# Kernel tuning notes

Hardware: AMD Instinct MI355X
Metric: run time of the kernel (lower is better)

## Reference

```python
import jax, jax.numpy as jnp
import numpy as np

DIM = 128
HEADS = 4
HEAD_DIM = DIM // HEADS
WS = (8, 8)
N = WS[0] * WS[1]
B = 4096
SCALE = HEAD_DIM ** -0.5


def _relative_position_index():
    # Swin-style relative position index, [N, N] int
    ch = np.arange(WS[0]); cw = np.arange(WS[1])
    coords = np.stack(np.meshgrid(ch, cw, indexing='ij'))          # [2, ws0, ws1]
    flat = coords.reshape(2, -1)                                    # [2, N]
    rel = flat[:, :, None] - flat[:, None, :]                       # [2, N, N]
    rel = rel.transpose(1, 2, 0)                                    # [N, N, 2]
    rel[:, :, 0] += WS[0] - 1
    rel[:, :, 1] += WS[1] - 1
    rel[:, :, 0] *= 2 * WS[1] - 1
    return jnp.asarray(rel.sum(-1))

REL_IDX = _relative_position_index()


def setup_inputs() -> dict:
    key = jax.random.key(0)
    ks = jax.random.split(key, 16)
    def lin(k, din, dout):
        return jax.random.normal(k, (din, dout), jnp.float32) * (din ** -0.5)
    return {
        'x': jax.random.normal(ks[0], (B, N, DIM), jnp.float32),
        'f': jax.random.normal(ks[1], (B, N, DIM), jnp.float32),
        'wq': lin(ks[2], DIM, DIM), 'bq': jnp.zeros((DIM,), jnp.float32),
        'wkv': lin(ks[3], DIM, 2 * DIM), 'bkv': jnp.zeros((2 * DIM,), jnp.float32),
        'wq_f': lin(ks[4], DIM, DIM), 'bq_f': jnp.zeros((DIM,), jnp.float32),
        'wkv_f': lin(ks[5], DIM, 2 * DIM), 'bkv_f': jnp.zeros((2 * DIM,), jnp.float32),
        'bias_table': jax.random.normal(ks[6], ((2 * WS[0] - 1) * (2 * WS[1] - 1), HEADS), jnp.float32) * 0.02,
        'wproj': lin(ks[7], DIM, DIM), 'bproj': jnp.zeros((DIM,), jnp.float32),
    }


def _qkv(t, wq, bq, wkv, bkv):
    Bn, Nn, C = t.shape
    q = (t @ wq + bq).reshape(Bn, Nn, HEADS, HEAD_DIM).transpose(0, 2, 1, 3)   # [B,H,N,D]
    kv = (t @ wkv + bkv).reshape(Bn, Nn, 2, HEADS, HEAD_DIM).transpose(2, 0, 3, 1, 4)
    return q, kv[0], kv[1]


def reference(x, f, wq, bq, wkv, bkv, wq_f, bq_f, wkv_f, bkv_f, bias_table, wproj, bproj):
    q, k, v = _qkv(x, wq, bq, wkv, bkv)
    attn = jnp.einsum('bhnd,bhmd->bhnm', q * SCALE, k)              # [B,H,N,N]
    q_f, k_f, _ = _qkv(f, wq_f, bq_f, wkv_f, bkv_f)
    attn_f = jnp.einsum('bhnd,bhmd->bhnm', q_f * SCALE, k_f)

    bias = bias_table[REL_IDX.reshape(-1)].reshape(N, N, HEADS)     # gather
    bias = bias.transpose(2, 0, 1)                                   # [H,N,N]
    ratio = attn.shape[-1] // bias.shape[-1]
    if ratio > 1:  # repeat last axis (no-op here since N == ws0*ws1)
        bias = jnp.repeat(bias, ratio, axis=-1)

    attn = (attn + bias[None]) * (attn_f + bias[None])               # joint modulation
    attn = jax.nn.softmax(attn, axis=-1)
    out = jnp.einsum('bhnm,bhmd->bhnd', attn, v)                     # [B,H,N,D]
    out = out.transpose(0, 2, 1, 3).reshape(x.shape[0], N, DIM)
    return out @ wproj + bproj
```

## Files before the change

### kernel.cpp

```cpp
#include <hip/hip_runtime.h>

typedef unsigned short u16;
typedef _Float16  f16x8  __attribute__((ext_vector_type(8)));
typedef _Float16  f16x4  __attribute__((ext_vector_type(4)));
typedef float     f32x4  __attribute__((ext_vector_type(4)));

#define MFMA_F16(a,b,c)  __builtin_amdgcn_mfma_f32_16x16x32_f16(a,b,c,0,0,0)

#define NTOK 64
#define DIM_ 128
#define SCALE_ 0.17677669529663687f

__device__ __forceinline__ u16 f2h_u(float x) {
    _Float16 h = (_Float16)x;
    return __builtin_bit_cast(u16, h);
}

__global__ void wja_prep(const float* __restrict__ wq, const float* __restrict__ wkv,
                         const float* __restrict__ wq_f, const float* __restrict__ wkv_f,
                         const float* __restrict__ wproj, u16* __restrict__ ws)
{
    const int blk = blockIdx.x;
    const int l = threadIdx.x;
    const float* W; int ldw, colbase;
    if (blk < 32)       { W = wq;    ldw = 128; colbase = (blk      >> 2) * 16; }
    else if (blk < 96)  { W = wkv;   ldw = 256; colbase = ((blk- 32) >> 2) * 16; }
    else if (blk < 128) { W = wq_f;  ldw = 128; colbase = ((blk- 96) >> 2) * 16; }
    else if (blk < 160) { W = wkv_f; ldw = 256; colbase = ((blk-128) >> 2) * 16; }
    else                { W = wproj; ldw = 128; colbase = ((blk-160) >> 2) * 16; }
    const int ks = blk & 3;
    const int m = l & 15, g = l >> 4;
    u16* dst = ws + blk * 512 + l * 8;
    #pragma unroll
    for (int i = 0; i < 8; ++i)
        dst[i] = f2h_u(W[(size_t)(32*ks + 8*g + i) * ldw + colbase + m]);
}

__global__ __launch_bounds__(256, 2)
void wja_fused(
    const float* __restrict__ x, const float* __restrict__ f,
    const float* __restrict__ bq, const float* __restrict__ bkv,
    const float* __restrict__ bq_f, const float* __restrict__ bkv_f,
    const float* __restrict__ bproj, const float* __restrict__ btab,
    const u16* __restrict__ ws, float* __restrict__ out)
{
    __shared__ __align__(16) u16 smem[27136];
    const int b    = blockIdx.x;
    const int tid  = threadIdx.x;
    const int w    = tid >> 6;
    const int lane = tid & 63;
    const int g    = lane >> 4;
    const int c    = lane & 15;
    const f32x4 zf4 = {0.f, 0.f, 0.f, 0.f};

    u16* const hq = smem + w * 4608;
    u16* const hk = hq + 2304;
    u16* const hv = smem + 18432 + w * 2176;

    const float* const xb = x + (size_t)b * (NTOK * DIM_);
    const float* const fb = f + (size_t)b * (NTOK * DIM_);

    auto ldf16 = [](const float* p) -> f16x8 {
        f16x8 r;
        #pragma unroll
        for (int i = 0; i < 8; ++i) r[i] = (_Float16)p[i];
        return r;
    };
    auto ldlds8 = [](const u16* p) -> f16x8 {
        struct P2 { f16x4 lo, hi; } t;
        t.lo = *(const f16x4*)p;
        t.hi = *(const f16x4*)(p + 4);
        return __builtin_bit_cast(f16x8, t);
    };

    auto gemmA = [&](const f16x8* afr, int wbase, const float* biasv, int which) {
        #pragma unroll
        for (int lct = 0; lct < 8; ++lct) {
            f32x4 acc = zf4;
            #pragma unroll
            for (int ks = 0; ks < 4; ++ks) {
                f16x8 bfr = *(const f16x8*)(ws + (wbase + 4*lct + ks) * 512 + lane * 8);
                acc = MFMA_F16(afr[ks], bfr, acc);
            }
            float bv = biasv[16*lct + c];
            const int hh = lct >> 1;
            const int cc = ((lct & 1) << 4) + c;
            #pragma unroll
            for (int i = 0; i < 4; ++i) {
                int row = 16*w + 4*g + i;
                u16 vv = f2h_u(acc[i] + bv);
                if (which == 0)      smem[hh*4608 + row*36 + cc] = vv;
                else if (which == 1) smem[hh*4608 + 2304 + row*36 + cc] = vv;
                else                 smem[18432 + hh*2176 + cc*68 + row] = vv;
            }
        }
    };

    {
        f16x8 xfr[4];
        #pragma unroll
        for (int ks = 0; ks < 4; ++ks)
            xfr[ks] = ldf16(xb + (16*w + c) * DIM_ + 32*ks + 8*g);
        gemmA(xfr,   0, bq,        0);
        gemmA(xfr,  32, bkv,       1);
        gemmA(xfr,  64, bkv + 128, 2);
    }
    __syncthreads();

    f32x4 S[4][4];
    {
        f16x8 qfr[4], kfr[4];
        #pragma unroll
        for (int t = 0; t < 4; ++t) {
            qfr[t] = ldlds8(hq + (16*t + c) * 36 + 8*g);
            kfr[t] = ldlds8(hk + (16*t + c) * 36 + 8*g);
        }
        #pragma unroll
        for (int mt = 0; mt < 4; ++mt)
            #pragma unroll
            for (int nt = 0; nt < 4; ++nt)
                S[mt][nt] = MFMA_F16(qfr[mt], kfr[nt], zf4);
    }
    __syncthreads();

    {
        f16x8 ffr[4];
        #pragma unroll
        for (int ks = 0; ks < 4; ++ks)
            ffr[ks] = ldf16(fb + (16*w + c) * DIM_ + 32*ks + 8*g);
        gemmA(ffr,  96, bq_f,  0);
        gemmA(ffr, 128, bkv_f, 1);
    }
    __syncthreads();

    {
        f16x8 kfr[4];
        #pragma unroll
        for (int t = 0; t < 4; ++t)
            kfr[t] = ldlds8(hk + (16*t + c) * 36 + 8*g);
        #pragma unroll
        for (int mt = 0; mt < 4; ++mt) {
            f16x8 qfr = ldlds8(hq + (16*mt + c) * 36 + 8*g);
            #pragma unroll
            for (int nt = 0; nt < 4; ++nt) {
                f32x4 sf = MFMA_F16(qfr, kfr[nt], zf4);
                int j = 16*nt + c;
                #pragma unroll
                for (int i = 0; i < 4; ++i) {
                    int r = 16*mt + 4*g + i;
                    int idx = ((r >> 3) - (j >> 3) + 7) * 15 + ((r & 7) - (j & 7) + 7);
                    float bv = btab[idx * 4 + w];
                    S[mt][nt][i] = (S[mt][nt][i] * SCALE_ + bv) * (sf[i] * SCALE_ + bv);
                }
            }
        }
    }

    float rmax[4][4], rinv[4][4];
    #pragma unroll
    for (int mt = 0; mt < 4; ++mt)
        #pragma unroll
        for (int i = 0; i < 4; ++i) {
            float m = fmaxf(fmaxf(S[mt][0][i], S[mt][1][i]), fmaxf(S[mt][2][i], S[mt][3][i]));
            #pragma unroll
            for (int d = 1; d < 16; d <<= 1) m = fmaxf(m, __shfl_xor(m, d));
            rmax[mt][i] = m;
        }
    #pragma unroll
    for (int mt = 0; mt < 4; ++mt)
        #pragma unroll
        for (int i = 0; i < 4; ++i) {
            float s0 = 0.f;
            #pragma unroll
            for (int nt = 0; nt < 4; ++nt) {
                float e = __expf(S[mt][nt][i] - rmax[mt][i]);
                S[mt][nt][i] = e;
                s0 += e;
            }
            #pragma unroll
            for (int d = 1; d < 16; d <<= 1) s0 += __shfl_xor(s0, d);
            rinv[mt][i] = 1.0f / s0;
        }

    #pragma unroll
    for (int mt = 0; mt < 4; ++mt)
        #pragma unroll
        for (int nt = 0; nt < 4; ++nt)
            #pragma unroll
            for (int i = 0; i < 4; ++i)
                hq[(16*mt + 4*g + i) * 72 + 16*nt + c] = f2h_u(S[mt][nt][i] * rinv[mt][i]);

    f32x4 O[4][2] = { { zf4, zf4 }, { zf4, zf4 }, { zf4, zf4 }, { zf4, zf4 } };
    #pragma unroll
    for (int ks = 0; ks < 2; ++ks) {
        f16x8 pfr[4], vfr[2];
        #pragma unroll
        for (int mt = 0; mt < 4; ++mt)
            pfr[mt] = *(const f16x8*)(hq + (16*mt + c) * 72 + 32*ks + 8*g);
        #pragma unroll
        for (int nt = 0; nt < 2; ++nt)
            vfr[nt] = ldlds8(hv + (16*nt + c) * 68 + 32*ks + 8*g);
        #pragma unroll
        for (int mt = 0; mt < 4; ++mt)
            #pragma unroll
            for (int nt = 0; nt < 2; ++nt)
                O[mt][nt] = MFMA_F16(pfr[mt], vfr[nt], O[mt][nt]);
    }

    #pragma unroll
    for (int mt = 0; mt < 4; ++mt)
        #pragma unroll
        for (int nt = 0; nt < 2; ++nt)
            #pragma unroll
            for (int i = 0; i < 4; ++i)
                hq[(16*mt + 4*g + i) * 40 + 16*nt + c] = f2h_u(O[mt][nt][i]);

    __syncthreads();

    f32x4 PO[4][2] = { { zf4, zf4 }, { zf4, zf4 }, { zf4, zf4 }, { zf4, zf4 } };
    #pragma unroll
    for (int ks = 0; ks < 4; ++ks) {
        const u16* ao = smem + ks * 4608;
        f16x8 afr[4];
        #pragma unroll
        for (int mt = 0; mt < 4; ++mt)
            afr[mt] = *(const f16x8*)(ao + (16*mt + c) * 40 + 8*g);
        #pragma unroll
        for (int lct = 0; lct < 2; ++lct) {
            f16x8 bfr = *(const f16x8*)(ws + (160 + (2*w + lct) * 4 + ks) * 512 + lane * 8);
            #pragma unroll
            for (int mt = 0; mt < 4; ++mt)
                PO[mt][lct] = MFMA_F16(afr[mt], bfr, PO[mt][lct]);
        }
    }
    __syncthreads();

    float* const fin = (float*)smem;
    #pragma unroll
    for (int lct = 0; lct < 2; ++lct) {
        float bv = bproj[32*w + 16*lct + c];
        #pragma unroll
        for (int mt = 0; mt < 4; ++mt)
            #pragma unroll
            for (int i = 0; i < 4; ++i)
                fin[(16*mt + 4*g + i) * 132 + 32*w + 16*lct + c] = PO[mt][lct][i] + bv;
    }
    __syncthreads();

    {
        const int row = tid >> 2, cb = (tid & 3) * 32;
        float* gout = out + (size_t)b * 8192 + row * 128 + cb;
        const float* src = fin + row * 132 + cb;
        #pragma unroll
        for (int q2 = 0; q2 < 8; ++q2)
            *(f32x4*)(gout + q2 * 4) = *(const f32x4*)(src + q2 * 4);
    }
}

extern "C" void kernel_launch(void* const* d_in, const int* in_sizes, int n_in,
                              void* d_out, int out_size, void* d_ws, size_t ws_size,
                              hipStream_t stream)
{
    const float* x     = (const float*)d_in[0];
    const float* f     = (const float*)d_in[1];
    const float* wq    = (const float*)d_in[2];
    const float* bq    = (const float*)d_in[3];
    const float* wkv   = (const float*)d_in[4];
    const float* bkv   = (const float*)d_in[5];
    const float* wq_f  = (const float*)d_in[6];
    const float* bq_f  = (const float*)d_in[7];
    const float* wkv_f = (const float*)d_in[8];
    const float* bkv_f = (const float*)d_in[9];
    const float* btab  = (const float*)d_in[10];
    const float* wproj = (const float*)d_in[11];
    const float* bproj = (const float*)d_in[12];
    u16* ws    = (u16*)d_ws;
    float* out = (float*)d_out;

    hipLaunchKernelGGL(wja_prep, dim3(192), dim3(64), 0, stream,
                       wq, wkv, wq_f, wkv_f, wproj, ws);
    hipLaunchKernelGGL(wja_fused, dim3(4096), dim3(256), 0, stream,
                       x, f, bq, bkv, bq_f, bkv_f, bproj, btab, ws, out);
}
```

Measured before the change: 217.1 us.

## Repack LDS per-head regions with tighter strides and hoist f loads

Reorganizes shared memory into one contiguous region per head (Q, K, transposed V), with smaller padded strides and a smaller total LDS allocation. Stores and loads to LDS use narrower 4-byte pieces where the new strides break 8-byte alignment. Global loads of both x and f are issued at kernel start so the f load latency overlaps the first projection. The hoisted loads raise register pressure, and the narrower LDS accesses raise the instruction count.

```diff
diff --git a/kernel.cpp b/kernel.cpp
--- a/kernel.cpp
+++ b/kernel.cpp
@@ -10,6 +10,15 @@
 #define NTOK 64
 #define DIM_ 128
 #define SCALE_ 0.17677669529663687f
+
+#define HREG 6464
+#define KOFF 2176
+#define VOFF 4352
+#define SQK  34
+#define SP   68
+#define SAO  36
+#define SVT  66
+#define SMEM_U16 25856
 
 __device__ __forceinline__ u16 f2h_u(float x) {
     _Float16 h = (_Float16)x;
@@ -44,7 +53,7 @@
     const float* __restrict__ bproj, const float* __restrict__ btab,
     const u16* __restrict__ ws, float* __restrict__ out)
 {
-    __shared__ __align__(16) u16 smem[27136];
+    __shared__ __align__(16) u16 smem[SMEM_U16];
     const int b    = blockIdx.x;
     const int tid  = threadIdx.x;
     const int w    = tid >> 6;
@@ -53,9 +62,7 @@
     const int c    = lane & 15;
     const f32x4 zf4 = {0.f, 0.f, 0.f, 0.f};
 
-    u16* const hq = smem + w * 4608;
-    u16* const hk = hq + 2304;
-    u16* const hv = smem + 18432 + w * 2176;
+    u16* const hb = smem + w * HREG;
 
     const float* const xb = x + (size_t)b * (NTOK * DIM_);
     const float* const fb = f + (size_t)b * (NTOK * DIM_);
@@ -72,6 +79,21 @@
         t.hi = *(const f16x4*)(p + 4);
         return __builtin_bit_cast(f16x8, t);
     };
+    auto ldlds4 = [](const u16* p) -> f16x8 {
+        struct P4 { unsigned a, b, c, d; } t;
+        t.a = *(const unsigned*)(p);
+        t.b = *(const unsigned*)(p + 2);
+        t.c = *(const unsigned*)(p + 4);
+        t.d = *(const unsigned*)(p + 6);
+        return __builtin_bit_cast(f16x8, t);
+    };
+
+    f16x8 xfr[4], ffr[4];
+    #pragma unroll
+    for (int ks = 0; ks < 4; ++ks) {
+        xfr[ks] = ldf16(xb + (16*w + c) * DIM_ + 32*ks + 8*g);
+        ffr[ks] = ldf16(fb + (16*w + c) * DIM_ + 32*ks + 8*g);
+    }
 
     auto gemmA = [&](const f16x8* afr, int wbase, const float* biasv, int which) {
         #pragma unroll
@@ -89,22 +111,16 @@
             for (int i = 0; i < 4; ++i) {
                 int row = 16*w + 4*g + i;
                 u16 vv = f2h_u(acc[i] + bv);
-                if (which == 0)      smem[hh*4608 + row*36 + cc] = vv;
-                else if (which == 1) smem[hh*4608 + 2304 + row*36 + cc] = vv;
-                else                 smem[18432 + hh*2176 + cc*68 + row] = vv;
-            }
-        }
-    };
-
-    {
-        f16x8 xfr[4];
-        #pragma unroll
-        for (int ks = 0; ks < 4; ++ks)
-            xfr[ks] = ldf16(xb + (16*w + c) * DIM_ + 32*ks + 8*g);
-        gemmA(xfr,   0, bq,        0);
-        gemmA(xfr,  32, bkv,       1);
-        gemmA(xfr,  64, bkv + 128, 2);
-    }
+                if (which == 0)      smem[hh*HREG + row*SQK + cc] = vv;
+                else if (which == 1) smem[hh*HREG + KOFF + row*SQK + cc] = vv;
+                else                 smem[hh*HREG + VOFF + cc*SVT + row] = vv;
+            }
+        }
+    };
+
+    gemmA(xfr,   0, bq,        0);
+    gemmA(xfr,  32, bkv,       1);
+    gemmA(xfr,  64, bkv + 128, 2);
     __syncthreads();
 
     f32x4 S[4][4];
@@ -112,8 +128,8 @@
         f16x8 qfr[4], kfr[4];
         #pragma unroll
         for (int t = 0; t < 4; ++t) {
-            qfr[t] = ldlds8(hq + (16*t + c) * 36 + 8*g);
-            kfr[t] = ldlds8(hk + (16*t + c) * 36 + 8*g);
+            qfr[t] = ldlds4(hb + (16*t + c) * SQK + 8*g);
+            kfr[t] = ldlds4(hb + KOFF + (16*t + c) * SQK + 8*g);
         }
         #pragma unroll
         for (int mt = 0; mt < 4; ++mt)
@@ -123,24 +139,18 @@
     }
     __syncthreads();
 
-    {
-        f16x8 ffr[4];
-        #pragma unroll
-        for (int ks = 0; ks < 4; ++ks)
-            ffr[ks] = ldf16(fb + (16*w + c) * DIM_ + 32*ks + 8*g);
-        gemmA(ffr,  96, bq_f,  0);
-        gemmA(ffr, 128, bkv_f, 1);
-    }
+    gemmA(ffr,  96, bq_f,  0);
+    gemmA(ffr, 128, bkv_f, 1);
     __syncthreads();
 
     {
         f16x8 kfr[4];
         #pragma unroll
         for (int t = 0; t < 4; ++t)
-            kfr[t] = ldlds8(hk + (16*t + c) * 36 + 8*g);
+            kfr[t] = ldlds4(hb + KOFF + (16*t + c) * SQK + 8*g);
         #pragma unroll
         for (int mt = 0; mt < 4; ++mt) {
-            f16x8 qfr = ldlds8(hq + (16*mt + c) * 36 + 8*g);
+            f16x8 qfr = ldlds4(hb + (16*mt + c) * SQK + 8*g);
             #pragma unroll
             for (int nt = 0; nt < 4; ++nt) {
                 f32x4 sf = MFMA_F16(qfr, kfr[nt], zf4);
@@ -188,7 +198,7 @@
         for (int nt = 0; nt < 4; ++nt)
             #pragma unroll
             for (int i = 0; i < 4; ++i)
-                hq[(16*mt + 4*g + i) * 72 + 16*nt + c] = f2h_u(S[mt][nt][i] * rinv[mt][i]);
+                hb[(16*mt + 4*g + i) * SP + 16*nt + c] = f2h_u(S[mt][nt][i] * rinv[mt][i]);
 
     f32x4 O[4][2] = { { zf4, zf4 }, { zf4, zf4 }, { zf4, zf4 }, { zf4, zf4 } };
     #pragma unroll
@@ -196,10 +206,10 @@
         f16x8 pfr[4], vfr[2];
         #pragma unroll
         for (int mt = 0; mt < 4; ++mt)
-            pfr[mt] = *(const f16x8*)(hq + (16*mt + c) * 72 + 32*ks + 8*g);
+            pfr[mt] = ldlds8(hb + (16*mt + c) * SP + 32*ks + 8*g);
         #pragma unroll
         for (int nt = 0; nt < 2; ++nt)
-            vfr[nt] = ldlds8(hv + (16*nt + c) * 68 + 32*ks + 8*g);
+            vfr[nt] = ldlds4(hb + VOFF + (16*nt + c) * SVT + 32*ks + 8*g);
         #pragma unroll
         for (int mt = 0; mt < 4; ++mt)
             #pragma unroll
@@ -213,18 +223,18 @@
         for (int nt = 0; nt < 2; ++nt)
             #pragma unroll
             for (int i = 0; i < 4; ++i)
-                hq[(16*mt + 4*g + i) * 40 + 16*nt + c] = f2h_u(O[mt][nt][i]);
+                hb[(16*mt + 4*g + i) * SAO + 16*nt + c] = f2h_u(O[mt][nt][i]);
 
     __syncthreads();
 
     f32x4 PO[4][2] = { { zf4, zf4 }, { zf4, zf4 }, { zf4, zf4 }, { zf4, zf4 } };
     #pragma unroll
     for (int ks = 0; ks < 4; ++ks) {
-        const u16* ao = smem + ks * 4608;
+        const u16* ao = smem + ks * HREG;
         f16x8 afr[4];
         #pragma unroll
         for (int mt = 0; mt < 4; ++mt)
-            afr[mt] = *(const f16x8*)(ao + (16*mt + c) * 40 + 8*g);
+            afr[mt] = ldlds8(ao + (16*mt + c) * SAO + 8*g);
         #pragma unroll
         for (int lct = 0; lct < 2; ++lct) {
             f16x8 bfr = *(const f16x8*)(ws + (160 + (2*w + lct) * 4 + ks) * 512 + lane * 8);
```

Measured after the change: 222.6 us. 1.03x slower.
